# Optimization experiments

Measured on AMD Instinct MI355X. Metric: run time of the kernel, lower is better.

Reference implementation:

```python
import jax, jax.numpy as jnp
import numpy as np

STDDEV = 8.0

def setup_inputs() -> dict:
    key = jax.random.key(0)
    k1, k2, k3, k4 = jax.random.split(key, 4)
    B, S, D, O = 32, 4096, 1024, 1024
    source_hidden_sequence = jax.random.normal(k1, (B, S, D), dtype=jnp.float32)
    target_hidden = jax.random.normal(k2, (B, D), dtype=jnp.float32)
    positions = jax.random.randint(k3, (B,), 0, S, dtype=jnp.int32)
    attention_weights = jax.random.normal(k4, (D + D, O), dtype=jnp.float32) * 0.02
    return {
        "source_hidden_sequence": source_hidden_sequence,
        "target_hidden": target_hidden,
        "positions": positions,
        "attention_weights": attention_weights,
    }

def reference(source_hidden_sequence, target_hidden, positions, attention_weights):
    # source_hidden_sequence: [B, S, D]; target_hidden: [B, D]; positions: [B]
    S = source_hidden_sequence.shape[1]
    # dot-product score per source position: [B, S]
    score = jnp.einsum('bsd,bd->bs', source_hidden_sequence, target_hidden)
    weights = jax.nn.softmax(score, axis=1)
    # Gaussian local-position decay centered at positions
    rel = jnp.arange(S, dtype=jnp.float32)[None, :] - positions.astype(jnp.float32)[:, None]  # [B, S]
    pos_w = jnp.exp(-(rel * rel) / (2.0 * STDDEV * STDDEV))
    weights = weights * pos_w
    # weighted sum over source sequence: [B, D]
    weighted = jnp.einsum('bsd,bs->bd', source_hidden_sequence, weights)
    combined = jnp.concatenate([target_hidden, weighted], axis=1)  # [B, 2D]
    return jnp.tanh(combined @ attention_weights)
```

## Files before the change

### kernel.cpp

```cpp
#include <hip/hip_runtime.h>

#define BB 32
#define SS 4096
#define DD 1024
#define OO 1024
#define KK 2048
#define RAD 64
#define NSPLIT 8
#define NBLK (SS / 16)

typedef float f4 __attribute__((ext_vector_type(4)));

__device__ __forceinline__ float dot4(f4 a, f4 q) {
  return a.x * q.x + a.y * q.y + a.z * q.z + a.w * q.w;
}

__global__ __launch_bounds__(256) void k_score(const float* __restrict__ src,
                                               const float* __restrict__ tgt,
                                               float* __restrict__ score,
                                               float* __restrict__ blkstats) {
  const int b = blockIdx.y;
  const int wave = threadIdx.x >> 6;
  const int lane = threadIdx.x & 63;
  const int s_base = blockIdx.x * 16 + wave * 4;

  const f4* tv = (const f4*)(tgt + (size_t)b * DD);
  f4 q0 = tv[lane], q1 = tv[64 + lane], q2 = tv[128 + lane], q3 = tv[192 + lane];

  const f4* r0 = (const f4*)(src + ((size_t)b * SS + s_base) * DD) + lane;
  const f4* r1 = r0 + 256;
  const f4* r2 = r0 + 512;
  const f4* r3 = r0 + 768;

  f4 a00 = __builtin_nontemporal_load(r0);
  f4 a01 = __builtin_nontemporal_load(r0 + 64);
  f4 a02 = __builtin_nontemporal_load(r0 + 128);
  f4 a03 = __builtin_nontemporal_load(r0 + 192);
  f4 a10 = __builtin_nontemporal_load(r1);
  f4 a11 = __builtin_nontemporal_load(r1 + 64);
  f4 a12 = __builtin_nontemporal_load(r1 + 128);
  f4 a13 = __builtin_nontemporal_load(r1 + 192);
  f4 a20 = __builtin_nontemporal_load(r2);
  f4 a21 = __builtin_nontemporal_load(r2 + 64);
  f4 a22 = __builtin_nontemporal_load(r2 + 128);
  f4 a23 = __builtin_nontemporal_load(r2 + 192);
  f4 a30 = __builtin_nontemporal_load(r3);
  f4 a31 = __builtin_nontemporal_load(r3 + 64);
  f4 a32 = __builtin_nontemporal_load(r3 + 128);
  f4 a33 = __builtin_nontemporal_load(r3 + 192);

  float p0 = (dot4(a00, q0) + dot4(a01, q1)) + (dot4(a02, q2) + dot4(a03, q3));
  float p1 = (dot4(a10, q0) + dot4(a11, q1)) + (dot4(a12, q2) + dot4(a13, q3));
  float p2 = (dot4(a20, q0) + dot4(a21, q1)) + (dot4(a22, q2) + dot4(a23, q3));
  float p3 = (dot4(a30, q0) + dot4(a31, q1)) + (dot4(a32, q2) + dot4(a33, q3));

  for (int off = 32; off > 0; off >>= 1) {
    p0 += __shfl_xor(p0, off);
    p1 += __shfl_xor(p1, off);
    p2 += __shfl_xor(p2, off);
    p3 += __shfl_xor(p3, off);
  }

  float sel = (lane == 0) ? p0 : ((lane == 1) ? p1 : ((lane == 2) ? p2 : p3));
  if (lane < 4) score[(size_t)b * SS + s_base + lane] = sel;

  __shared__ float rowv[16];
  if (lane < 4) rowv[wave * 4 + lane] = sel;
  __syncthreads();
  if (threadIdx.x == 0) {
    float m = rowv[0];
    #pragma unroll
    for (int i = 1; i < 16; ++i) m = fmaxf(m, rowv[i]);
    float l = 0.f;
    #pragma unroll
    for (int i = 0; i < 16; ++i) l += expf(rowv[i] - m);
    float* bs = blkstats + ((size_t)b * NBLK + blockIdx.x) * 2;
    bs[0] = m; bs[1] = l;
  }
}

__global__ __launch_bounds__(256) void k_combine(const float* __restrict__ blkstats,
                                                 float* __restrict__ stats) {
  const int b = blockIdx.x;
  const int wave = threadIdx.x >> 6;
  const int lane = threadIdx.x & 63;
  const float* bs = blkstats + ((size_t)b * NBLK + threadIdx.x) * 2;
  float m = bs[0];
  float l = bs[1];
  for (int off = 32; off > 0; off >>= 1) {
    float m2 = __shfl_xor(m, off);
    float l2 = __shfl_xor(l, off);
    float mm = fmaxf(m, m2);
    l = l * expf(m - mm) + l2 * expf(m2 - mm);
    m = mm;
  }
  __shared__ float sm[4], sl[4];
  if (lane == 0) { sm[wave] = m; sl[wave] = l; }
  __syncthreads();
  if (threadIdx.x == 0) {
    float M = fmaxf(fmaxf(sm[0], sm[1]), fmaxf(sm[2], sm[3]));
    float L = sl[0] * expf(sm[0] - M) + sl[1] * expf(sm[1] - M) +
              sl[2] * expf(sm[2] - M) + sl[3] * expf(sm[3] - M);
    stats[2 * b] = M;
    stats[2 * b + 1] = L;
  }
}

__global__ __launch_bounds__(256) void k_weighted(const float* __restrict__ src,
                                                  const float* __restrict__ score,
                                                  const float* __restrict__ stats,
                                                  const int* __restrict__ pos,
                                                  float* __restrict__ partial) {
  const int b = blockIdx.y;
  const int split = blockIdx.x;
  const int p = pos[b];
  int w0 = p - RAD; if (w0 < 0) w0 = 0;
  int w1 = p + RAD + 1; if (w1 > SS) w1 = SS;
  const int len = w1 - w0;
  const int chunk = (len + NSPLIT - 1) / NSPLIT;
  int cs = w0 + split * chunk;
  int ce = cs + chunk; if (ce > w1) ce = w1;
  const float m = stats[2 * b];
  const float inv = 1.f / stats[2 * b + 1];
  const int t = threadIdx.x;
  float a0 = 0.f, a1 = 0.f, a2 = 0.f, a3 = 0.f;
  for (int s = cs; s < ce; ++s) {
    float rel = (float)(s - p);
    float w = expf(score[(size_t)b * SS + s] - m) * inv * expf(rel * rel * (-1.f / 128.f));
    f4 v = ((const f4*)(src + ((size_t)b * SS + s) * DD))[t];
    a0 += w * v.x; a1 += w * v.y; a2 += w * v.z; a3 += w * v.w;
  }
  f4* outp = (f4*)(partial + ((size_t)split * BB + b) * DD);
  f4 o; o.x = a0; o.y = a1; o.z = a2; o.w = a3;
  outp[t] = o;
}

__global__ __launch_bounds__(256) void k_out(const float* __restrict__ tgt,
                                             const float* __restrict__ partial,
                                             const float* __restrict__ W,
                                             float* __restrict__ out) {
  const int b = blockIdx.y;
  const int o0 = blockIdx.x * 128;
  __shared__ float c[KK];
  __shared__ float red[4][128];
  for (int k = threadIdx.x; k < KK; k += 256) {
    float v;
    if (k < DD) {
      v = tgt[(size_t)b * DD + k];
    } else {
      const int d = k - DD;
      v = 0.f;
      for (int pp = 0; pp < NSPLIT; ++pp) v += partial[((size_t)pp * BB + b) * DD + d];
    }
    c[k] = v;
  }
  __syncthreads();
  const int ks = threadIdx.x >> 6;
  const int ol = threadIdx.x & 63;
  float acc0 = 0.f, acc1 = 0.f;
  const float* wp = W + o0 + ol * 2;
  for (int k = ks * 512; k < ks * 512 + 512; ++k) {
    float2 wv = *(const float2*)(wp + (size_t)k * OO);
    float ck = c[k];
    acc0 += ck * wv.x; acc1 += ck * wv.y;
  }
  red[ks][ol * 2] = acc0;
  red[ks][ol * 2 + 1] = acc1;
  __syncthreads();
  if (threadIdx.x < 128) {
    float s = red[0][threadIdx.x] + red[1][threadIdx.x] + red[2][threadIdx.x] + red[3][threadIdx.x];
    out[(size_t)b * OO + o0 + threadIdx.x] = tanhf(s);
  }
}

extern "C" void kernel_launch(void* const* d_in, const int* in_sizes, int n_in,
                              void* d_out, int out_size, void* d_ws, size_t ws_size,
                              hipStream_t stream) {
  const float* src = (const float*)d_in[0];
  const float* tgt = (const float*)d_in[1];
  const int* pos   = (const int*)d_in[2];
  const float* W   = (const float*)d_in[3];
  float* out = (float*)d_out;

  float* ws       = (float*)d_ws;
  float* score    = ws;
  float* stats    = score + (size_t)BB * SS;
  float* partial  = stats + 2 * BB;
  float* blkstats = partial + (size_t)NSPLIT * BB * DD;

  k_score   <<<dim3(SS / 16, BB), 256, 0, stream>>>(src, tgt, score, blkstats);
  k_combine <<<BB,                256, 0, stream>>>(blkstats, stats);
  k_weighted<<<dim3(NSPLIT, BB),  256, 0, stream>>>(src, score, stats, pos, partial);
  k_out     <<<dim3(OO / 128, BB), 256, 0, stream>>>(tgt, partial, W, out);
}
```

Before: 687.4 us.

## Fuse softmax stat combine into weighted kernel and batch-tile output GEMM

Removes the separate k_combine launch by having every k_weighted block redo the per-batch max/sum reduction over the block stats. NSPLIT drops from 8 to 4. The output projection is restructured so each block handles all 32 batches for a 16-column slice, with the weights and combined inputs staged through shared memory in K tiles. The point is to read W once instead of once per batch. The trade-off is fewer, longer-running blocks (64) in k_out, and each weighted block repeating the reduction.

```diff
diff --git a/kernel.cpp b/kernel.cpp
--- a/kernel.cpp
+++ b/kernel.cpp
@@ -4,12 +4,15 @@
 #define SS 4096
 #define DD 1024
 #define OO 1024
-#define KK 2048
 #define RAD 64
-#define NSPLIT 8
+#define NSPLIT 4
 #define NBLK (SS / 16)
+#define OTILE 16
+#define KTILE 256
+#define NKT ((DD + DD) / KTILE)
 
 typedef float f4 __attribute__((ext_vector_type(4)));
+typedef float f2 __attribute__((ext_vector_type(2)));
 
 __device__ __forceinline__ float dot4(f4 a, f4 q) {
   return a.x * q.x + a.y * q.y + a.z * q.z + a.w * q.w;
@@ -79,14 +82,19 @@
   }
 }
 
-__global__ __launch_bounds__(256) void k_combine(const float* __restrict__ blkstats,
-                                                 float* __restrict__ stats) {
-  const int b = blockIdx.x;
+__global__ __launch_bounds__(256) void k_weighted(const float* __restrict__ src,
+                                                  const float* __restrict__ score,
+                                                  const float* __restrict__ blkstats,
+                                                  const int* __restrict__ pos,
+                                                  float* __restrict__ partial) {
+  const int b = blockIdx.y;
+  const int split = blockIdx.x;
   const int wave = threadIdx.x >> 6;
   const int lane = threadIdx.x & 63;
-  const float* bs = blkstats + ((size_t)b * NBLK + threadIdx.x) * 2;
-  float m = bs[0];
-  float l = bs[1];
+
+  const float* bs = blkstats + (size_t)b * NBLK * 2;
+  float m = bs[2 * threadIdx.x];
+  float l = bs[2 * threadIdx.x + 1];
   for (int off = 32; off > 0; off >>= 1) {
     float m2 = __shfl_xor(m, off);
     float l2 = __shfl_xor(l, off);
@@ -97,22 +105,11 @@
   __shared__ float sm[4], sl[4];
   if (lane == 0) { sm[wave] = m; sl[wave] = l; }
   __syncthreads();
-  if (threadIdx.x == 0) {
-    float M = fmaxf(fmaxf(sm[0], sm[1]), fmaxf(sm[2], sm[3]));
-    float L = sl[0] * expf(sm[0] - M) + sl[1] * expf(sm[1] - M) +
-              sl[2] * expf(sm[2] - M) + sl[3] * expf(sm[3] - M);
-    stats[2 * b] = M;
-    stats[2 * b + 1] = L;
-  }
-}
-
-__global__ __launch_bounds__(256) void k_weighted(const float* __restrict__ src,
-                                                  const float* __restrict__ score,
-                                                  const float* __restrict__ stats,
-                                                  const int* __restrict__ pos,
-                                                  float* __restrict__ partial) {
-  const int b = blockIdx.y;
-  const int split = blockIdx.x;
+  const float M = fmaxf(fmaxf(sm[0], sm[1]), fmaxf(sm[2], sm[3]));
+  const float L = sl[0] * expf(sm[0] - M) + sl[1] * expf(sm[1] - M) +
+                  sl[2] * expf(sm[2] - M) + sl[3] * expf(sm[3] - M);
+  const float inv = 1.f / L;
+
   const int p = pos[b];
   int w0 = p - RAD; if (w0 < 0) w0 = 0;
   int w1 = p + RAD + 1; if (w1 > SS) w1 = SS;
@@ -120,13 +117,12 @@
   const int chunk = (len + NSPLIT - 1) / NSPLIT;
   int cs = w0 + split * chunk;
   int ce = cs + chunk; if (ce > w1) ce = w1;
-  const float m = stats[2 * b];
-  const float inv = 1.f / stats[2 * b + 1];
+
   const int t = threadIdx.x;
   float a0 = 0.f, a1 = 0.f, a2 = 0.f, a3 = 0.f;
   for (int s = cs; s < ce; ++s) {
     float rel = (float)(s - p);
-    float w = expf(score[(size_t)b * SS + s] - m) * inv * expf(rel * rel * (-1.f / 128.f));
+    float w = expf(score[(size_t)b * SS + s] - M) * inv * expf(rel * rel * (-1.f / 128.f));
     f4 v = ((const f4*)(src + ((size_t)b * SS + s) * DD))[t];
     a0 += w * v.x; a1 += w * v.y; a2 += w * v.z; a3 += w * v.w;
   }
@@ -139,38 +135,53 @@
                                              const float* __restrict__ partial,
                                              const float* __restrict__ W,
                                              float* __restrict__ out) {
-  const int b = blockIdx.y;
-  const int o0 = blockIdx.x * 128;
-  __shared__ float c[KK];
-  __shared__ float red[4][128];
-  for (int k = threadIdx.x; k < KK; k += 256) {
-    float v;
-    if (k < DD) {
-      v = tgt[(size_t)b * DD + k];
+  const int o0 = blockIdx.x * OTILE;
+  __shared__ float ct[32][KTILE + 1];
+  __shared__ f2 wt[KTILE][OTILE / 2];
+  const int tid = threadIdx.x;
+  const int bown = tid & 31;
+  const int opair = tid >> 5;
+  float acc0 = 0.f, acc1 = 0.f;
+
+  for (int kt = 0; kt < NKT; ++kt) {
+    const int k0 = kt * KTILE;
+    __syncthreads();
+    if (k0 < DD) {
+      for (int idx = tid; idx < 32 * KTILE; idx += 256) {
+        const int bb = idx >> 8;
+        const int kk = idx & (KTILE - 1);
+        ct[bb][kk] = tgt[(size_t)bb * DD + k0 + kk];
+      }
     } else {
-      const int d = k - DD;
-      v = 0.f;
-      for (int pp = 0; pp < NSPLIT; ++pp) v += partial[((size_t)pp * BB + b) * DD + d];
+      const int kd0 = k0 - DD;
+      for (int idx = tid; idx < 32 * KTILE; idx += 256) {
+        const int bb = idx >> 8;
+        const int kk = idx & (KTILE - 1);
+        const size_t base = (size_t)bb * DD + kd0 + kk;
+        float v = partial[base] +
+                  partial[(size_t)1 * BB * DD + base] +
+                  partial[(size_t)2 * BB * DD + base] +
+                  partial[(size_t)3 * BB * DD + base];
+        ct[bb][kk] = v;
+      }
     }
-    c[k] = v;
-  }
-  __syncthreads();
-  const int ks = threadIdx.x >> 6;
-  const int ol = threadIdx.x & 63;
-  float acc0 = 0.f, acc1 = 0.f;
-  const float* wp = W + o0 + ol * 2;
-  for (int k = ks * 512; k < ks * 512 + 512; ++k) {
-    float2 wv = *(const float2*)(wp + (size_t)k * OO);
-    float ck = c[k];
-    acc0 += ck * wv.x; acc1 += ck * wv.y;
-  }
-  red[ks][ol * 2] = acc0;
-  red[ks][ol * 2 + 1] = acc1;
-  __syncthreads();
-  if (threadIdx.x < 128) {
-    float s = red[0][threadIdx.x] + red[1][threadIdx.x] + red[2][threadIdx.x] + red[3][threadIdx.x];
-    out[(size_t)b * OO + o0 + threadIdx.x] = tanhf(s);
-  }
+    for (int idx = tid; idx < KTILE * (OTILE / 2); idx += 256) {
+      const int row = idx >> 3;
+      const int c2 = idx & 7;
+      wt[row][c2] = *(const f2*)(W + (size_t)(k0 + row) * OO + o0 + c2 * 2);
+    }
+    __syncthreads();
+    #pragma unroll 8
+    for (int kk = 0; kk < KTILE; ++kk) {
+      float c = ct[bown][kk];
+      f2 w = wt[kk][opair];
+      acc0 += c * w.x;
+      acc1 += c * w.y;
+    }
+  }
+  const int o = o0 + opair * 2;
+  out[(size_t)bown * OO + o]     = tanhf(acc0);
+  out[(size_t)bown * OO + o + 1] = tanhf(acc1);
 }
 
 extern "C" void kernel_launch(void* const* d_in, const int* in_sizes, int n_in,
@@ -184,12 +195,10 @@
 
   float* ws       = (float*)d_ws;
   float* score    = ws;
-  float* stats    = score + (size_t)BB * SS;
-  float* partial  = stats + 2 * BB;
-  float* blkstats = partial + (size_t)NSPLIT * BB * DD;
+  float* blkstats = score + (size_t)BB * SS;
+  float* partial  = blkstats + (size_t)BB * NBLK * 2;
 
   k_score   <<<dim3(SS / 16, BB), 256, 0, stream>>>(src, tgt, score, blkstats);
-  k_combine <<<BB,                256, 0, stream>>>(blkstats, stats);
-  k_weighted<<<dim3(NSPLIT, BB),  256, 0, stream>>>(src, score, stats, pos, partial);
-  k_out     <<<dim3(OO / 128, BB), 256, 0, stream>>>(tgt, partial, W, out);
-}
+  k_weighted<<<dim3(NSPLIT, BB),  256, 0, stream>>>(src, score, blkstats, pos, partial);
+  k_out     <<<dim3(OO / OTILE, 1), 256, 0, stream>>>(tgt, partial, W, out);
+}
```

After: 722.9 us. +5.2%, slower.
